# Kernel optimization log

Measured on AMD Instinct MI355X. Metric: run time of the kernel, lower is better.

## Reference

```python
import jax, jax.numpy as jnp
import numpy as np

N_Q = 5  # generalized coordinates of the AMBER 5-link biped
N_U = 4  # actuated joints

# Constant actuation matrix (underactuated first joint).
_B_CONST = np.array([[0., 0., 0., 0.],
                     [1., 0., 0., 0.],
                     [0., 1., 0., 0.],
                     [0., 0., 1., 0.],
                     [0., 0., 0., 1.]], dtype=np.float32)


def D_matrix(q):
    """Surrogate SPD mass matrix, trig-structured like the codegen'd original.
    q: [B, 5] -> [B, 5, 5]."""
    cosdiff = jnp.cos(q[:, :, None] - q[:, None, :])  # [B,5,5]
    return 2.0 * jnp.eye(N_Q, dtype=q.dtype) + 0.3 * cosdiff


def H_vector(q, qdot):
    """Surrogate Coriolis + gravity + damping vector. -> [B, 5, 1]."""
    v2 = jnp.sum(qdot * qdot, axis=1, keepdims=True)  # [B,1]
    h = 0.1 * jnp.sin(q) * v2 + 9.8 * jnp.sin(q) + 0.05 * qdot  # [B,5]
    return h[:, :, None]


def B_matrix(q):
    """Actuation matrix broadcast over batch. -> [B, 5, 4]."""
    return jnp.broadcast_to(jnp.asarray(_B_CONST, q.dtype), (q.shape[0], N_Q, N_U))


def setup_inputs() -> dict:
    key = jax.random.key(0)
    k1, k2 = jax.random.split(key)
    B = 1_000_000
    state = jax.random.normal(k1, (B, 10), dtype=jnp.float32)
    u = jax.random.normal(k2, (B, N_U, 1), dtype=jnp.float32)
    t = jnp.zeros((1,), dtype=jnp.float32)  # unused ODE time
    return {"t": t, "state": state, "u": u}


def reference(t, state, u):
    # xddot = f(state) + g(state) @ u
    q = state[:, :5]      # [B,5]
    qdot = state[:, 5:10]  # [B,5]
    D = D_matrix(q)                    # [B,5,5]
    H = H_vector(q, qdot)              # [B,5,1]
    Bm = B_matrix(q)                   # [B,5,4]
    Dinv = jnp.linalg.inv(D)           # th.inverse(D); reused for H and B
    f = jnp.concatenate([qdot[:, :, None], -(Dinv @ H)], axis=1)  # [B,10,1]
    g = jnp.concatenate([jnp.zeros_like(Bm), Dinv @ Bm], axis=1)  # [B,10,4]
    return f + g @ u                   # [B,10,1]
```

## Files before the change

### kernel.cpp

```cpp
#include <hip/hip_runtime.h>

#define NQ 5

__global__ __launch_bounds__(256) void amber_dyn_kernel(
    const float* __restrict__ state,
    const float* __restrict__ u,
    float* __restrict__ out,
    int B)
{
    int idx = blockIdx.x * blockDim.x + threadIdx.x;
    if (idx >= B) return;

    const float2* st2 = reinterpret_cast<const float2*>(state + (size_t)idx * 10);
    float2 r0 = st2[0], r1 = st2[1], r2 = st2[2], r3 = st2[3], r4 = st2[4];
    float q[5]  = {r0.x, r0.y, r1.x, r1.y, r2.x};
    float qd[5] = {r2.y, r3.x, r3.y, r4.x, r4.y};

    float4 uv = reinterpret_cast<const float4*>(u)[idx];

    float s[5], c[5];
    #pragma unroll
    for (int i = 0; i < 5; ++i) __sincosf(q[i], &s[i], &c[i]);

    float v2 = qd[0]*qd[0] + qd[1]*qd[1] + qd[2]*qd[2] + qd[3]*qd[3] + qd[4]*qd[4];
    float coef = 0.1f * v2 + 9.8f;

    float bu[5] = {0.f, uv.x, uv.y, uv.z, uv.w};
    float rhs[5];
    #pragma unroll
    for (int i = 0; i < 5; ++i)
        rhs[i] = bu[i] - (coef * s[i] + 0.05f * qd[i]);

    float D[5][5];
    #pragma unroll
    for (int i = 0; i < 5; ++i) {
        #pragma unroll
        for (int j = 0; j < 5; ++j) {
            float v = 0.3f * (c[i]*c[j] + s[i]*s[j]);
            D[i][j] = (i == j) ? (v + 2.0f) : v;
        }
    }

    #pragma unroll
    for (int k = 0; k < 5; ++k) {
        float inv = 1.0f / D[k][k];
        #pragma unroll
        for (int r = k + 1; r < 5; ++r) {
            float m = D[r][k] * inv;
            #pragma unroll
            for (int cc = k + 1; cc < 5; ++cc)
                D[r][cc] -= m * D[k][cc];
            rhs[r] -= m * rhs[k];
        }
    }
    float x[5];
    #pragma unroll
    for (int k = 4; k >= 0; --k) {
        float acc = rhs[k];
        #pragma unroll
        for (int cc = k + 1; cc < 5; ++cc) acc -= D[k][cc] * x[cc];
        x[k] = acc / D[k][k];
    }

    float2* o2 = reinterpret_cast<float2*>(out + (size_t)idx * 10);
    o2[0] = make_float2(qd[0], qd[1]);
    o2[1] = make_float2(qd[2], qd[3]);
    o2[2] = make_float2(qd[4], x[0]);
    o2[3] = make_float2(x[1],  x[2]);
    o2[4] = make_float2(x[3],  x[4]);
}

extern "C" void kernel_launch(void* const* d_in, const int* in_sizes, int n_in,
                              void* d_out, int out_size, void* d_ws, size_t ws_size,
                              hipStream_t stream) {
    const float* state = (const float*)d_in[1];
    const float* u     = (const float*)d_in[2];
    float* out = (float*)d_out;
    int B = in_sizes[1] / 10;

    int block = 256;
    int grid = (B + block - 1) / block;
    amber_dyn_kernel<<<grid, block, 0, stream>>>(state, u, out, B);
}
```

Baseline: 23.01 us.

## Replace 5x5 Gaussian elimination with Woodbury rank-2 closed-form solve

```diff
diff --git a/kernel.cpp b/kernel.cpp
--- a/kernel.cpp
+++ b/kernel.cpp
@@ -1,6 +1,6 @@
 #include <hip/hip_runtime.h>
 
-#define NQ 5
+__device__ __forceinline__ float frcp(float x) { return __builtin_amdgcn_rcpf(x); }
 
 __global__ __launch_bounds__(256) void amber_dyn_kernel(
     const float* __restrict__ state,
@@ -26,41 +26,34 @@
     float coef = 0.1f * v2 + 9.8f;
 
     float bu[5] = {0.f, uv.x, uv.y, uv.z, uv.w};
-    float rhs[5];
+    float r[5];
     #pragma unroll
     for (int i = 0; i < 5; ++i)
-        rhs[i] = bu[i] - (coef * s[i] + 0.05f * qd[i]);
+        r[i] = bu[i] - (coef * s[i] + 0.05f * qd[i]);
 
-    float D[5][5];
+    float cc = 0.f, cs = 0.f, pc = 0.f, ps = 0.f;
     #pragma unroll
     for (int i = 0; i < 5; ++i) {
-        #pragma unroll
-        for (int j = 0; j < 5; ++j) {
-            float v = 0.3f * (c[i]*c[j] + s[i]*s[j]);
-            D[i][j] = (i == j) ? (v + 2.0f) : v;
-        }
+        cc += c[i] * c[i];
+        cs += c[i] * s[i];
+        pc += c[i] * r[i];
+        ps += s[i] * r[i];
     }
+    float ss = 5.0f - cc;
 
-    #pragma unroll
-    for (int k = 0; k < 5; ++k) {
-        float inv = 1.0f / D[k][k];
-        #pragma unroll
-        for (int r = k + 1; r < 5; ++r) {
-            float m = D[r][k] * inv;
-            #pragma unroll
-            for (int cc = k + 1; cc < 5; ++cc)
-                D[r][cc] -= m * D[k][cc];
-            rhs[r] -= m * rhs[k];
-        }
-    }
+    const float K = 10.0f / 3.0f;
+    float m00 = K + 0.5f * cc;
+    float m01 = 0.5f * cs;
+    float m11 = K + 0.5f * ss;
+
+    float idet = frcp(m00 * m11 - m01 * m01);
+    float y0 = 0.25f * idet * (m11 * pc - m01 * ps);
+    float y1 = 0.25f * idet * (m00 * ps - m01 * pc);
+
     float x[5];
     #pragma unroll
-    for (int k = 4; k >= 0; --k) {
-        float acc = rhs[k];
-        #pragma unroll
-        for (int cc = k + 1; cc < 5; ++cc) acc -= D[k][cc] * x[cc];
-        x[k] = acc / D[k][k];
-    }
+    for (int i = 0; i < 5; ++i)
+        x[i] = 0.5f * r[i] - (c[i] * y0 + s[i] * y1);
 
     float2* o2 = reinterpret_cast<float2*>(out + (size_t)idx * 10);
     o2[0] = make_float2(qd[0], qd[1]);
```

Measured after the change: 21.68 us. -5.8%, faster.
